# Kernel tuning notes

Measured on AMD Instinct MI355X. Metric: run time of the kernel, lower is better.

The kernel has to match this reference:

```python
import jax, jax.numpy as jnp
import numpy as np

EPS_NORM = 1e-12  # F.normalize eps
EPS_BN = 1e-5     # BatchNorm1d eps


def _gather_neighbors(tensor, index):
    # tensor: (bs, v, d), index: (bs, v, n) -> (bs, v, n, d)
    return jax.vmap(lambda t, i: t[i])(tensor, index)


def setup_inputs() -> dict:
    key = jax.random.key(0)
    ks = jax.random.split(key, 8)
    bs, v, n = 4, 4096, 32
    cin, cout = 128, 256
    stdv = float(np.sqrt(2.0 / cout))
    return {
        "neighbor_index": jax.random.randint(ks[0], (bs, v, n), 0, v),
        "vertices": jax.random.normal(ks[1], (bs, v, 3), dtype=jnp.float32),
        "feature_map": jax.random.normal(ks[2], (bs, v, cin - 1), dtype=jnp.float32),
        "directions": jax.random.uniform(ks[3], (4, cout), minval=-stdv, maxval=stdv, dtype=jnp.float32),
        "W": jax.random.normal(ks[4], (cout, cin), dtype=jnp.float32) / np.sqrt(cin),
        "b": jnp.zeros((cout,), jnp.float32),
        "gamma": jnp.ones((cout,), jnp.float32),
        "beta": jnp.zeros((cout,), jnp.float32),
    }


def reference(neighbor_index, vertices, feature_map, directions, W, b, gamma, beta):
    # --- direction-based weights theta: (bs, v, n, cout) ---
    neighbors = _gather_neighbors(vertices, neighbor_index)          # (bs,v,n,3)
    direc = neighbors - vertices[:, :, None, :]
    direc_norm = direc / jnp.maximum(
        jnp.linalg.norm(direc, axis=-1, keepdims=True), EPS_NORM)    # F.normalize
    dir_w = (direc_norm + 1.0) * 0.5                                  # (bs,v,n,3)
    sup_w = jnp.stack([directions[1] - directions[0],
                       directions[2] - directions[0],
                       directions[3] - directions[0]], axis=0)        # (3, cout)
    theta = jax.nn.relu(jnp.einsum('bvnk,kc->bvnc', dir_w, sup_w) + directions[0])

    # --- gathered features + L2 distance channel ---
    fs = _gather_neighbors(feature_map, neighbor_index)               # (bs,v,n,cin-1)
    fdist = jnp.sqrt(jnp.sum(fs * fs, axis=-1, keepdims=True))        # (bs,v,n,1)
    fs = jnp.concatenate([fs, fdist], axis=-1)                        # (bs,v,n,cin)

    # --- Linear -> BatchNorm1d (training stats) -> ReLU ---
    z = jnp.einsum('bvni,ci->bvnc', fs, W) + b                        # (bs,v,n,cout)
    mean = jnp.mean(z, axis=(0, 1, 2))
    var = jnp.mean(jnp.square(z - mean), axis=(0, 1, 2))              # biased var
    zn = (z - mean) * jax.lax.rsqrt(var + EPS_BN) * gamma + beta
    act = jax.nn.relu(zn) * theta

    # --- max-pool over neighbor dim ---
    return jnp.max(act, axis=2)                                       # (bs,v,cout)
```

## Files before the change

### kernel.cpp

```cpp
#include <hip/hip_runtime.h>

typedef unsigned short ushort_t;
typedef __attribute__((ext_vector_type(8))) short short8;
typedef __attribute__((ext_vector_type(4))) float floatx4;
typedef __attribute__((ext_vector_type(2))) float floatx2;

#define NN    32
#define CIN   128
#define COUT  256
#define NPTS  16384
#define NSAMP (NPTS * NN)
#define LDA   136
#define YBLK  256

__device__ ushort_t g_wb[COUT * CIN];
__device__ ushort_t g_y[(size_t)NPTS * COUT];
__device__ int      g_mult[NPTS];
__device__ float    g_stat[512];
__device__ float    g_consts[1536];
__device__ int      g_done;

__device__ __forceinline__ float bf2f(ushort_t u) {
    return __uint_as_float(((unsigned int)u) << 16);
}
__device__ __forceinline__ ushort_t f2bf(float f) {
    unsigned int x = __float_as_uint(f);
    return (ushort_t)((x + 0x7FFFu + ((x >> 16) & 1u)) >> 16);
}

__global__ void hist_kernel(const float* __restrict__ Wg,
                            const int* __restrict__ nbr) {
    const int tid = threadIdx.x;
    if (blockIdx.x < 32) {
        int i = blockIdx.x * 1024 + tid * 4;
        float4 v = ((const float4*)Wg)[i >> 2];
        g_wb[i] = f2bf(v.x); g_wb[i + 1] = f2bf(v.y);
        g_wb[i + 2] = f2bf(v.z); g_wb[i + 3] = f2bf(v.w);
    }
    int gid = blockIdx.x * 256 + tid;
    int gv  = ((gid >> 17) << 12) + nbr[gid];
    atomicAdd(&g_mult[gv], 1);
}

__global__ __launch_bounds__(256, 2)
void ygemm_kernel(const float* __restrict__ fm,
                  const float* __restrict__ gamma,
                  const float* __restrict__ beta,
                  const float* __restrict__ dirs) {
    __shared__ ushort_t At[64 * LDA];
    __shared__ float    multS[64];
    __shared__ int      lastS;

    const int tid  = threadIdx.x;
    const int r0   = blockIdx.x * 64;
    const int lane = tid & 63;
    const int wv   = tid >> 6;

    if (tid < 64) multS[tid] = (float)g_mult[r0 + tid];

    #pragma unroll
    for (int i = 0; i < 16; ++i) {
        int rloc = wv * 16 + i;
        const float* src = fm + (size_t)(r0 + rloc) * 127;
        float f0 = src[lane];
        float f1 = (lane < 63) ? src[64 + lane] : 0.0f;
        float ss = f0 * f0 + f1 * f1;
        #pragma unroll
        for (int d = 1; d < 64; d <<= 1) ss += __shfl_xor(ss, d, 64);
        float fd = sqrtf(ss);
        At[rloc * LDA + lane]      = f2bf(f0);
        At[rloc * LDA + 64 + lane] = (lane < 63) ? f2bf(f1) : f2bf(fd);
    }
    __syncthreads();

    if (tid < 64) g_mult[r0 + tid] = 0;

    const int m = lane & 15;
    const int q = lane >> 4;

    floatx4 acc[4][4];
    #pragma unroll
    for (int rt = 0; rt < 4; ++rt)
        #pragma unroll
        for (int ct = 0; ct < 4; ++ct)
            acc[rt][ct] = (floatx4){0.0f, 0.0f, 0.0f, 0.0f};

    #pragma unroll
    for (int kk = 0; kk < 4; ++kk) {
        const int kof = kk * 32 + q * 8;
        short8 af[4];
        #pragma unroll
        for (int rt = 0; rt < 4; ++rt)
            af[rt] = *(const short8*)&At[(rt * 16 + m) * LDA + kof];
        short8 bfr[4];
        #pragma unroll
        for (int ct = 0; ct < 4; ++ct) {
            int ch = wv * 64 + ct * 16 + m;
            bfr[ct] = *(const short8*)(g_wb + ch * CIN + kof);
        }
        #pragma unroll
        for (int rt = 0; rt < 4; ++rt)
            #pragma unroll
            for (int ct = 0; ct < 4; ++ct)
                acc[rt][ct] = __builtin_amdgcn_mfma_f32_16x16x32_bf16(
                    af[rt], bfr[ct], acc[rt][ct], 0, 0, 0);
    }

    #pragma unroll
    for (int ct = 0; ct < 4; ++ct) {
        const int ch = wv * 64 + ct * 16 + m;
        float s = 0.0f, ss = 0.0f;
        #pragma unroll
        for (int rt = 0; rt < 4; ++rt)
            #pragma unroll
            for (int j = 0; j < 4; ++j) {
                int rloc = rt * 16 + q * 4 + j;
                ushort_t yb = f2bf(acc[rt][ct][j]);
                g_y[(size_t)(r0 + rloc) * COUT + ch] = yb;
                float yv = bf2f(yb);
                float wm = multS[rloc];
                s  += wm * yv;
                ss += wm * yv * yv;
            }
        s  += __shfl_xor(s, 16, 64);  s  += __shfl_xor(s, 32, 64);
        ss += __shfl_xor(ss, 16, 64); ss += __shfl_xor(ss, 32, 64);
        if (q == 0) {
            atomicAdd(&g_stat[ch], s);
            atomicAdd(&g_stat[256 + ch], ss);
        }
    }

    __syncthreads();
    if (tid == 0) {
        __threadfence();
        int old = atomicAdd(&g_done, 1);
        lastS = (old == YBLK - 1) ? 1 : 0;
    }
    __syncthreads();
    if (lastS) {
        __threadfence();
        int c = tid;
        float sum = atomicAdd(&g_stat[c], 0.0f);
        float ssq = atomicAdd(&g_stat[256 + c], 0.0f);
        const float invN = 1.0f / (float)NSAMP;
        float mean = sum * invN;
        float var  = fmaxf(ssq * invN - mean * mean, 0.0f);
        float inv  = 1.0f / sqrtf(var + 1e-5f);
        float scale = gamma[c] * inv;
        g_consts[c]        = scale;
        g_consts[256 + c]  = beta[c] - mean * scale;
        float d0 = dirs[c];
        g_consts[512 + c]  = d0;
        g_consts[768 + c]  = dirs[256 + c] - d0;
        g_consts[1024 + c] = dirs[512 + c] - d0;
        g_consts[1280 + c] = dirs[768 + c] - d0;
        g_stat[c] = 0.0f; g_stat[256 + c] = 0.0f;
        if (tid == 0) g_done = 0;
    }
}

__global__ __launch_bounds__(128, 4)
void epi_kernel(const int* __restrict__ nbr,
                const float* __restrict__ verts,
                float* __restrict__ out) {
    __shared__ int    rows[NN];
    __shared__ float4 dws[NN];

    const int p   = blockIdx.x;
    const int tid = threadIdx.x;

    if (tid < NN) {
        int gv = ((p >> 12) << 12) + nbr[p * NN + tid];
        rows[tid] = gv;
        float dx = verts[gv * 3 + 0] - verts[p * 3 + 0];
        float dy = verts[gv * 3 + 1] - verts[p * 3 + 1];
        float dz = verts[gv * 3 + 2] - verts[p * 3 + 2];
        float nrm = sqrtf(dx * dx + dy * dy + dz * dz);
        float inv = 1.0f / fmaxf(nrm, 1e-12f);
        dws[tid] = make_float4((dx * inv + 1.0f) * 0.5f,
                               (dy * inv + 1.0f) * 0.5f,
                               (dz * inv + 1.0f) * 0.5f, 0.0f);
    }
    __syncthreads();

    const int c2 = tid * 2;
    const floatx2 zero = {0.0f, 0.0f};
    floatx2 sc = *(const floatx2*)&g_consts[c2];
    floatx2 sh = *(const floatx2*)&g_consts[256 + c2];
    floatx2 d0 = *(const floatx2*)&g_consts[512 + c2];
    floatx2 s0 = *(const floatx2*)&g_consts[768 + c2];
    floatx2 s1 = *(const floatx2*)&g_consts[1024 + c2];
    floatx2 s2 = *(const floatx2*)&g_consts[1280 + c2];

    floatx2 vm0 = zero, vm1 = zero, vm2 = zero, vm3 = zero;
    #pragma unroll
    for (int j = 0; j < NN; j += 4) {
        #pragma unroll
        for (int jj = 0; jj < 4; ++jj) {
            int rb = __builtin_amdgcn_readfirstlane(rows[j + jj]);
            const unsigned int* rp =
                (const unsigned int*)(g_y + (size_t)rb * COUT);
            unsigned int u = rp[tid];
            floatx2 y;
            y.x = __uint_as_float(u << 16);
            y.y = __uint_as_float(u & 0xFFFF0000u);
            float4 dw = dws[j + jj];
            floatx2 th = d0 + s0 * dw.x + s1 * dw.y + s2 * dw.z;
            th = __builtin_elementwise_max(th, zero);
            floatx2 zt = (y * sc + sh) * th;
            if      (jj == 0) vm0 = __builtin_elementwise_max(vm0, zt);
            else if (jj == 1) vm1 = __builtin_elementwise_max(vm1, zt);
            else if (jj == 2) vm2 = __builtin_elementwise_max(vm2, zt);
            else              vm3 = __builtin_elementwise_max(vm3, zt);
        }
    }
    floatx2 vm = __builtin_elementwise_max(
        __builtin_elementwise_max(vm0, vm1),
        __builtin_elementwise_max(vm2, vm3));

    *(floatx2*)(out + (size_t)p * COUT + c2) = vm;
}

extern "C" void kernel_launch(void* const* d_in, const int* in_sizes, int n_in,
                              void* d_out, int out_size, void* d_ws, size_t ws_size,
                              hipStream_t stream) {
    const int*   nbr   = (const int*)d_in[0];
    const float* verts = (const float*)d_in[1];
    const float* fm    = (const float*)d_in[2];
    const float* dirs  = (const float*)d_in[3];
    const float* Wg    = (const float*)d_in[4];
    const float* gamma = (const float*)d_in[6];
    const float* beta  = (const float*)d_in[7];
    (void)d_ws; (void)ws_size; (void)in_sizes; (void)n_in; (void)out_size;

    hist_kernel<<<dim3(NSAMP / 256), dim3(256), 0, stream>>>(Wg, nbr);
    ygemm_kernel<<<dim3(YBLK), dim3(256), 0, stream>>>(fm, gamma, beta, dirs);
    epi_kernel<<<dim3(NPTS), dim3(128), 0, stream>>>(nbr, verts, (float*)d_out);
}
```

Baseline: 170.0 us.

## Move feature bf16 conversion into prep kernel and split BN finalize out

The fp32-to-bf16 feature conversion and per-row L2 norm move out of the GEMM kernel into the histogram kernel, which now runs 4096 blocks and writes a padded bf16 feature buffer. The GEMM kernel then loads that buffer into shared memory with 16-byte copies. The last-block-done counter, threadfence and in-kernel batch-norm finalize are replaced by a separate single-block finalize kernel. This spreads the serial conversion across more of the GPU and removes atomic synchronisation, at the cost of an extra kernel launch and a round trip of the bf16 features through global memory.

Measured after the change: 156.1 us. -8.2%, faster.

```diff
diff --git a/kernel.cpp b/kernel.cpp
--- a/kernel.cpp
+++ b/kernel.cpp
@@ -11,14 +11,13 @@
 #define NPTS  16384
 #define NSAMP (NPTS * NN)
 #define LDA   136
-#define YBLK  256
-
+
+__device__ ushort_t g_fsp[(size_t)NPTS * 128];
 __device__ ushort_t g_wb[COUT * CIN];
 __device__ ushort_t g_y[(size_t)NPTS * COUT];
 __device__ int      g_mult[NPTS];
 __device__ float    g_stat[512];
 __device__ float    g_consts[1536];
-__device__ int      g_done;
 
 __device__ __forceinline__ float bf2f(ushort_t u) {
     return __uint_as_float(((unsigned int)u) << 16);
@@ -28,7 +27,8 @@
     return (ushort_t)((x + 0x7FFFu + ((x >> 16) & 1u)) >> 16);
 }
 
-__global__ void hist_kernel(const float* __restrict__ Wg,
+__global__ void prep_kernel(const float* __restrict__ fm,
+                            const float* __restrict__ Wg,
                             const int* __restrict__ nbr) {
     const int tid = threadIdx.x;
     if (blockIdx.x < 32) {
@@ -38,45 +38,50 @@
         g_wb[i + 2] = f2bf(v.z); g_wb[i + 3] = f2bf(v.w);
     }
     int gid = blockIdx.x * 256 + tid;
-    int gv  = ((gid >> 17) << 12) + nbr[gid];
-    atomicAdd(&g_mult[gv], 1);
+    if (gid < NSAMP) {
+        int gv = ((gid >> 17) << 12) + nbr[gid];
+        atomicAdd(&g_mult[gv], 1);
+    }
+    int row  = blockIdx.x * 4 + (tid >> 6);
+    int lane = tid & 63;
+    const float* src = fm + (size_t)row * 127;
+    float f0 = src[lane];
+    float f1 = (lane < 63) ? src[64 + lane] : 0.0f;
+    float ss = f0 * f0 + f1 * f1;
+    #pragma unroll
+    for (int d = 1; d < 64; d <<= 1) ss += __shfl_xor(ss, d, 64);
+    float fd = sqrtf(ss);
+    ushort_t* dst = g_fsp + (size_t)row * 128;
+    dst[lane]      = f2bf(f0);
+    dst[64 + lane] = (lane < 63) ? f2bf(f1) : f2bf(fd);
 }
 
 __global__ __launch_bounds__(256, 2)
-void ygemm_kernel(const float* __restrict__ fm,
-                  const float* __restrict__ gamma,
-                  const float* __restrict__ beta,
-                  const float* __restrict__ dirs) {
+void ygemm_kernel() {
     __shared__ ushort_t At[64 * LDA];
     __shared__ float    multS[64];
-    __shared__ int      lastS;
-
-    const int tid  = threadIdx.x;
-    const int r0   = blockIdx.x * 64;
+
+    const int tid = threadIdx.x;
+    const int r0  = blockIdx.x * 64;
+
+    if (tid < 64) {
+        multS[tid] = (float)g_mult[r0 + tid];
+        g_mult[r0 + tid] = 0;
+    }
+    #pragma unroll
+    for (int i = 0; i < 4; ++i) {
+        int chunk = tid + i * 256;
+        int r = chunk >> 4;
+        int c = chunk & 15;
+        const uint4 v = *(const uint4*)(g_fsp + (size_t)(r0 + r) * 128 + c * 8);
+        *(uint4*)&At[r * LDA + c * 8] = v;
+    }
+    __syncthreads();
+
     const int lane = tid & 63;
-    const int wv   = tid >> 6;
-
-    if (tid < 64) multS[tid] = (float)g_mult[r0 + tid];
-
-    #pragma unroll
-    for (int i = 0; i < 16; ++i) {
-        int rloc = wv * 16 + i;
-        const float* src = fm + (size_t)(r0 + rloc) * 127;
-        float f0 = src[lane];
-        float f1 = (lane < 63) ? src[64 + lane] : 0.0f;
-        float ss = f0 * f0 + f1 * f1;
-        #pragma unroll
-        for (int d = 1; d < 64; d <<= 1) ss += __shfl_xor(ss, d, 64);
-        float fd = sqrtf(ss);
-        At[rloc * LDA + lane]      = f2bf(f0);
-        At[rloc * LDA + 64 + lane] = (lane < 63) ? f2bf(f1) : f2bf(fd);
-    }
-    __syncthreads();
-
-    if (tid < 64) g_mult[r0 + tid] = 0;
-
-    const int m = lane & 15;
-    const int q = lane >> 4;
+    const int w    = tid >> 6;
+    const int m    = lane & 15;
+    const int q    = lane >> 4;
 
     floatx4 acc[4][4];
     #pragma unroll
@@ -95,7 +100,7 @@
         short8 bfr[4];
         #pragma unroll
         for (int ct = 0; ct < 4; ++ct) {
-            int ch = wv * 64 + ct * 16 + m;
+            int ch = w * 64 + ct * 16 + m;
             bfr[ct] = *(const short8*)(g_wb + ch * CIN + kof);
         }
         #pragma unroll
@@ -108,7 +113,7 @@
 
     #pragma unroll
     for (int ct = 0; ct < 4; ++ct) {
-        const int ch = wv * 64 + ct * 16 + m;
+        const int ch = w * 64 + ct * 16 + m;
         float s = 0.0f, ss = 0.0f;
         #pragma unroll
         for (int rt = 0; rt < 4; ++rt)
@@ -129,34 +134,25 @@
             atomicAdd(&g_stat[256 + ch], ss);
         }
     }
-
-    __syncthreads();
-    if (tid == 0) {
-        __threadfence();
-        int old = atomicAdd(&g_done, 1);
-        lastS = (old == YBLK - 1) ? 1 : 0;
-    }
-    __syncthreads();
-    if (lastS) {
-        __threadfence();
-        int c = tid;
-        float sum = atomicAdd(&g_stat[c], 0.0f);
-        float ssq = atomicAdd(&g_stat[256 + c], 0.0f);
-        const float invN = 1.0f / (float)NSAMP;
-        float mean = sum * invN;
-        float var  = fmaxf(ssq * invN - mean * mean, 0.0f);
-        float inv  = 1.0f / sqrtf(var + 1e-5f);
-        float scale = gamma[c] * inv;
-        g_consts[c]        = scale;
-        g_consts[256 + c]  = beta[c] - mean * scale;
-        float d0 = dirs[c];
-        g_consts[512 + c]  = d0;
-        g_consts[768 + c]  = dirs[256 + c] - d0;
-        g_consts[1024 + c] = dirs[512 + c] - d0;
-        g_consts[1280 + c] = dirs[768 + c] - d0;
-        g_stat[c] = 0.0f; g_stat[256 + c] = 0.0f;
-        if (tid == 0) g_done = 0;
-    }
+}
+
+__global__ void finalize_kernel(const float* __restrict__ gamma,
+                                const float* __restrict__ beta,
+                                const float* __restrict__ dirs) {
+    int c = threadIdx.x;
+    const float invN = 1.0f / (float)NSAMP;
+    float mean = g_stat[c] * invN;
+    float var  = fmaxf(g_stat[256 + c] * invN - mean * mean, 0.0f);
+    float inv  = 1.0f / sqrtf(var + 1e-5f);
+    g_stat[c] = 0.0f; g_stat[256 + c] = 0.0f;
+    float scale = gamma[c] * inv;
+    g_consts[c]        = scale;
+    g_consts[256 + c]  = beta[c] - mean * scale;
+    float d0 = dirs[c];
+    g_consts[512 + c]  = d0;
+    g_consts[768 + c]  = dirs[256 + c] - d0;
+    g_consts[1024 + c] = dirs[512 + c] - d0;
+    g_consts[1280 + c] = dirs[768 + c] - d0;
 }
 
 __global__ __launch_bounds__(128, 4)
@@ -233,7 +229,8 @@
     const float* beta  = (const float*)d_in[7];
     (void)d_ws; (void)ws_size; (void)in_sizes; (void)n_in; (void)out_size;
 
-    hist_kernel<<<dim3(NSAMP / 256), dim3(256), 0, stream>>>(Wg, nbr);
-    ygemm_kernel<<<dim3(YBLK), dim3(256), 0, stream>>>(fm, gamma, beta, dirs);
+    prep_kernel<<<dim3(NPTS / 4), dim3(256), 0, stream>>>(fm, Wg, nbr);
+    ygemm_kernel<<<dim3(NPTS / 64), dim3(256), 0, stream>>>();
+    finalize_kernel<<<dim3(1), dim3(256), 0, stream>>>(gamma, beta, dirs);
     epi_kernel<<<dim3(NPTS), dim3(128), 0, stream>>>(nbr, verts, (float*)d_out);
 }
```
